# Performance work log

Measured on AMD Instinct MI355X. Metric: run time of the kernel, lower is better.

Reference implementation:

```python
import jax, jax.numpy as jnp
import numpy as np

G, N, E = 32, 1024, 16384
F_IN, HID, OUT = 128, 1024, 4096
B, S, VOCAB = 32, 256, 32000


def sage_layer(x, src, dst, Wl, Wr, b):
    # x: [N, Fin]; mean-aggregate source features at destination nodes (PyG SAGEConv)
    agg = jax.ops.segment_sum(x[src], dst, num_segments=x.shape[0])
    cnt = jax.ops.segment_sum(jnp.ones(src.shape, x.dtype), dst, num_segments=x.shape[0])
    agg = agg / jnp.maximum(cnt, 1.0)[:, None]
    return agg @ Wl + x @ Wr + b  # lin_l(mean_neigh) + lin_r(x) + bias


def setup_inputs() -> dict:
    key = jax.random.key(0)
    ks = jax.random.split(key, 12)
    node_features = jax.random.normal(ks[0], (G, N, F_IN), dtype=jnp.float32)
    edge_index = jax.random.randint(ks[1], (G, 2, E), 0, N, dtype=jnp.int32)
    input_ids = jax.random.randint(ks[2], (B, S), 0, VOCAB, dtype=jnp.int32)
    is_node = jnp.zeros((B, S), dtype=bool).at[:, 0].set(True)  # one graph token per row -> G True entries
    s1 = 1.0 / np.sqrt(F_IN)
    s2 = 1.0 / np.sqrt(HID)
    Wl1 = jax.random.normal(ks[3], (F_IN, HID), jnp.float32) * s1
    Wr1 = jax.random.normal(ks[4], (F_IN, HID), jnp.float32) * s1
    b1 = jnp.zeros((HID,), jnp.float32)
    Wl2 = jax.random.normal(ks[5], (HID, OUT), jnp.float32) * s2
    Wr2 = jax.random.normal(ks[6], (HID, OUT), jnp.float32) * s2
    b2 = jnp.zeros((OUT,), jnp.float32)
    embed_tokens = jax.random.normal(ks[7], (VOCAB, OUT), jnp.float32) * 0.02
    return {"node_features": node_features, "edge_index": edge_index, "input_ids": input_ids,
            "is_node": is_node, "Wl1": Wl1, "Wr1": Wr1, "b1": b1, "Wl2": Wl2, "Wr2": Wr2,
            "b2": b2, "embed_tokens": embed_tokens}


def reference(node_features, edge_index, input_ids, is_node, Wl1, Wr1, b1, Wl2, Wr2, b2, embed_tokens):
    def gnn_one_graph(x, ei):
        src, dst = ei[0], ei[1]
        h = jax.nn.relu(sage_layer(x, src, dst, Wl1, Wr1, b1))  # dropout is identity at inference
        h = sage_layer(h, src, dst, Wl2, Wr2, b2)
        return h.mean(axis=0)  # global_mean_pool -> [OUT]; torch code then takes [0]

    graph_emb = jax.vmap(gnn_one_graph)(node_features, edge_index)  # [G, OUT]

    inputs_embeds = embed_tokens[input_ids]  # [B, S, OUT]
    d = inputs_embeds.shape[-1]
    flat_mask = is_node.reshape(-1)                      # [B*S]
    order = jnp.cumsum(flat_mask.astype(jnp.int32)) - 1  # k-th True -> graph k
    repl = graph_emb[jnp.clip(order, 0, graph_emb.shape[0] - 1)]  # [B*S, OUT]
    out = jnp.where(flat_mask[:, None], repl, inputs_embeds.reshape(-1, d))
    return out.reshape(inputs_embeds.shape)
```

## Files before the change

kernel.cpp:

```cpp
#include <hip/hip_runtime.h>
#include <hip/hip_bf16.h>
#include <stdint.h>

#define G 32
#define NN 1024
#define EE 16384
#define FIN 128
#define HID 1024
#define OUT 4096
#define BB 32
#define SS 256

typedef __bf16 bf16_t;
typedef __attribute__((ext_vector_type(8))) __bf16 bf16x8;
typedef __attribute__((ext_vector_type(4))) float f32x4;

#define WS_FLAG     0
#define WS_CNT      4096
#define WS_WNODE    135168
#define WS_HSUM     266240
#define WS_WSUM     397312
#define WS_EMB      528384
#define WS_ZERO_BYTES 1048576
#define WS_ROWPTR   1052672
#define WS_CURSOR   1183744
#define WS_POS2G    1314816
#define WS_B1F      1347584
#define WS_B2F      1351680
#define WS_ESRC     1368064
#define WS_XBF      3465216
#define WS_AGG      11853824
#define WS_WCATT    20242432

__device__ inline float ldf(const void* p, size_t i, int f32) {
    return f32 ? ((const float*)p)[i] : (float)((const bf16_t*)p)[i];
}

__global__ __launch_bounds__(256) void probe_dtype_k(const void* x, int* flag) {
    __shared__ int s;
    int t = threadIdx.x;
    if (t == 0) s = 0;
    __syncthreads();
    const unsigned short* u = (const unsigned short*)x;
    int bad = 0;
    for (int i = t; i < 4096; i += 256) {
        unsigned short h = u[2 * i];
        int e = (h >> 7) & 0xFF;
        if (e >= 0xC0) bad = 1;
    }
    if (bad) atomicAdd(&s, 1);
    __syncthreads();
    if (t == 0) *flag = (s > 0) ? 1 : 0;
}

__global__ __launch_bounds__(256) void conv_x_k(const void* x, const int* flag,
                                                bf16_t* __restrict__ xbf) {
    int f32 = *flag;
    size_t i = ((size_t)blockIdx.x * 256 + threadIdx.x) * 4;
    if (f32) {
        const float* xf = (const float*)x;
        bf16_t o0 = (bf16_t)xf[i], o1 = (bf16_t)xf[i + 1],
               o2 = (bf16_t)xf[i + 2], o3 = (bf16_t)xf[i + 3];
        unsigned short p[4] = {*(unsigned short*)&o0, *(unsigned short*)&o1,
                               *(unsigned short*)&o2, *(unsigned short*)&o3};
        *(uint2*)(xbf + i) = *(uint2*)p;
    } else {
        *(uint2*)(xbf + i) = *(const uint2*)((const bf16_t*)x + i);
    }
}

__global__ __launch_bounds__(256) void conv_b_k(const void* b1, const void* b2,
                                                const int* flag,
                                                float* __restrict__ b1f,
                                                float* __restrict__ b2f) {
    int f32 = *flag;
    int t = blockIdx.x * 256 + threadIdx.x;
    if (t < HID) b1f[t] = ldf(b1, t, f32);
    else if (t < HID + OUT) b2f[t - HID] = ldf(b2, t - HID, f32);
}

__global__ __launch_bounds__(256) void count_edges_k(const int* __restrict__ ei,
                                                     int* __restrict__ cnt) {
    int idx = blockIdx.x * 256 + threadIdx.x;
    int g = idx >> 14, e = idx & (EE - 1);
    int dst = ei[(g * 2 + 1) * EE + e];
    atomicAdd(&cnt[g * NN + dst], 1);
}

__global__ __launch_bounds__(256) void wnode_k(const int* __restrict__ ei,
                                               const int* __restrict__ cnt,
                                               float* __restrict__ wnode) {
    int idx = blockIdx.x * 256 + threadIdx.x;
    int g = idx >> 14, e = idx & (EE - 1);
    int src = ei[g * 2 * EE + e];
    int dst = ei[(g * 2 + 1) * EE + e];
    int c = cnt[g * NN + dst];
    float w = 1.0f / (float)(c > 1 ? c : 1);
    atomicAdd(&wnode[g * NN + src], w);
}

__global__ __launch_bounds__(256) void scan_rowptr_k(const int* __restrict__ cnt,
                                                     int* __restrict__ rowptr,
                                                     int* __restrict__ cursor) {
    int g = blockIdx.x;
    const int* c = cnt + g * NN;
    __shared__ int part[256];
    int t = threadIdx.x;
    int c0 = c[t * 4], c1 = c[t * 4 + 1], c2 = c[t * 4 + 2], c3 = c[t * 4 + 3];
    int s = c0 + c1 + c2 + c3;
    part[t] = s;
    __syncthreads();
    for (int off = 1; off < 256; off <<= 1) {
        int v = (t >= off) ? part[t - off] : 0;
        __syncthreads();
        part[t] += v;
        __syncthreads();
    }
    int base = part[t] - s;
    int gi = g * NN + t * 4;
    int o0 = base, o1 = o0 + c0, o2 = o1 + c1, o3 = o2 + c2;
    rowptr[gi] = o0; rowptr[gi + 1] = o1; rowptr[gi + 2] = o2; rowptr[gi + 3] = o3;
    cursor[gi] = o0; cursor[gi + 1] = o1; cursor[gi + 2] = o2; cursor[gi + 3] = o3;
}

__global__ __launch_bounds__(256) void scatter_edges_k(const int* __restrict__ ei,
                                                       int* __restrict__ cursor,
                                                       int* __restrict__ esrc) {
    int idx = blockIdx.x * 256 + threadIdx.x;
    int g = idx >> 14, e = idx & (EE - 1);
    int src = ei[g * 2 * EE + e];
    int dst = ei[(g * 2 + 1) * EE + e];
    int p = atomicAdd(&cursor[g * NN + dst], 1);
    esrc[g * EE + p] = src;
}

__global__ __launch_bounds__(256) void aggregate_k(const bf16_t* __restrict__ x,
                                                   const int* __restrict__ rowptr,
                                                   const int* __restrict__ cnt,
                                                   const int* __restrict__ esrc,
                                                   bf16_t* __restrict__ agg) {
    int g = blockIdx.x >> 9;
    int pair = blockIdx.x & 511;
    int n = pair * 2 + (threadIdx.x >> 7);
    int f = threadIdx.x & 127;
    int start = rowptr[g * NN + n];
    int deg = cnt[g * NN + n];
    const bf16_t* xg = x + (size_t)g * NN * FIN;
    const int* es = esrc + g * EE;
    float sum = 0.f;
    for (int i = 0; i < deg; ++i) {
        int s = es[start + i];
        sum += (float)xg[s * FIN + f];
    }
    float inv = 1.0f / (float)(deg > 1 ? deg : 1);
    agg[((size_t)g * NN + n) * FIN + f] = (bf16_t)(sum * inv);
}

__global__ __launch_bounds__(256) void build_wcatT_k(const void* Wl1, const void* Wr1,
                                                     const int* flag,
                                                     bf16_t* __restrict__ wcatT) {
    int f32 = *flag;
    int n = blockIdx.x;
    int k = threadIdx.x;
    float v = (k < 128) ? ldf(Wl1, (size_t)k * HID + n, f32)
                        : ldf(Wr1, (size_t)(k - 128) * HID + n, f32);
    wcatT[n * 256 + k] = (bf16_t)v;
}

#define BKP 40
__global__ __launch_bounds__(256) void l1_gemm_k(const bf16_t* __restrict__ agg,
                                                 const bf16_t* __restrict__ x,
                                                 const bf16_t* __restrict__ wcatT,
                                                 const float* __restrict__ b1f,
                                                 const float* __restrict__ wnode,
                                                 float* __restrict__ hsum,
                                                 float* __restrict__ wsum) {
    int nt = blockIdx.x, mt = blockIdx.y, g = blockIdx.z;
    __shared__ bf16_t As[128 * BKP];
    __shared__ bf16_t Bs[128 * BKP];
    int tid = threadIdx.x;
    int lane = tid & 63, wave = tid >> 6;
    int quad = lane >> 4, l16 = lane & 15;
    int m0 = (wave >> 1) * 64, n0 = (wave & 1) * 64;

    f32x4 acc[4][4] = {};
    const size_t arow = ((size_t)g * NN + (size_t)mt * 128) * FIN;

    for (int kc = 0; kc < 8; ++kc) {
        int k0 = kc * 32;
        const bf16_t* asrc = (k0 < 128) ? (agg + arow + k0) : (x + arow + (k0 - 128));
        const bf16_t* bsrc = wcatT + (size_t)(nt * 128) * 256 + k0;
        #pragma unroll
        for (int i = 0; i < 2; ++i) {
            int gi = tid + i * 256;
            int row = gi >> 2, col = (gi & 3) * 8;
            *(bf16x8*)(&As[row * BKP + col]) = *(const bf16x8*)(asrc + row * FIN + col);
            *(bf16x8*)(&Bs[row * BKP + col]) = *(const bf16x8*)(bsrc + row * 256 + col);
        }
        __syncthreads();
        bf16x8 a[4], b[4];
        int kl = quad * 8;
        #pragma unroll
        for (int t4 = 0; t4 < 4; ++t4) {
            a[t4] = *(const bf16x8*)(&As[(m0 + t4 * 16 + l16) * BKP + kl]);
            b[t4] = *(const bf16x8*)(&Bs[(n0 + t4 * 16 + l16) * BKP + kl]);
        }
        #pragma unroll
        for (int ti = 0; ti < 4; ++ti)
            #pragma unroll
            for (int tj = 0; tj < 4; ++tj)
                acc[ti][tj] = __builtin_amdgcn_mfma_f32_16x16x32_bf16(a[ti], b[tj], acc[ti][tj], 0, 0, 0);
        __syncthreads();
    }

    const float* wn = wnode + (size_t)g * NN + mt * 128;
    #pragma unroll
    for (int tj = 0; tj < 4; ++tj) {
        int ng = nt * 128 + n0 + tj * 16 + l16;
        float bias = b1f[ng];
        float hs = 0.f, wsv = 0.f;
        #pragma unroll
        for (int ti = 0; ti < 4; ++ti) {
            int mb = m0 + ti * 16 + quad * 4;
            #pragma unroll
            for (int r = 0; r < 4; ++r) {
                float h = acc[ti][tj][r] + bias;
                h = h > 0.f ? h : 0.f;
                hs += h;
                wsv += wn[mb + r] * h;
            }
        }
        hs += __shfl_xor(hs, 16);  hs += __shfl_xor(hs, 32);
        wsv += __shfl_xor(wsv, 16); wsv += __shfl_xor(wsv, 32);
        if (quad == 0) {
            atomicAdd(&hsum[(size_t)g * HID + ng], hs);
            atomicAdd(&wsum[(size_t)g * HID + ng], wsv);
        }
    }
}

__global__ __launch_bounds__(256) void l2_gemv_k(const float* __restrict__ wsum,
                                                 const float* __restrict__ hsum,
                                                 const void* Wl2v, const void* Wr2v,
                                                 const int* flag,
                                                 float* __restrict__ emb_acc) {
    int f32 = *flag;
    int jc = blockIdx.x;
    int kc = blockIdx.y;
    int t = threadIdx.x;
    int j = jc * 256 + t;
    __shared__ float u1[G][128];
    __shared__ float u2[G][128];
    for (int i = 0; i < 16; ++i) {
        int idx = t + i * 256;
        int g = idx >> 7, kk = idx & 127;
        u1[g][kk] = wsum[g * HID + kc * 128 + kk] * (1.0f / 1024.0f);
        u2[g][kk] = hsum[g * HID + kc * 128 + kk] * (1.0f / 1024.0f);
    }
    __syncthreads();
    float acc[G] = {};
    if (f32) {
        const float* L = (const float*)Wl2v;
        const float* R = (const float*)Wr2v;
        for (int kk = 0; kk < 128; ++kk) {
            size_t krow = (size_t)(kc * 128 + kk);
            float wl = L[krow * OUT + j];
            float wr = R[krow * OUT + j];
            #pragma unroll
            for (int g = 0; g < G; ++g)
                acc[g] = fmaf(u1[g][kk], wl, fmaf(u2[g][kk], wr, acc[g]));
        }
    } else {
        const bf16_t* L = (const bf16_t*)Wl2v;
        const bf16_t* R = (const bf16_t*)Wr2v;
        for (int kk = 0; kk < 128; ++kk) {
            size_t krow = (size_t)(kc * 128 + kk);
            float wl = (float)L[krow * OUT + j];
            float wr = (float)R[krow * OUT + j];
            #pragma unroll
            for (int g = 0; g < G; ++g)
                acc[g] = fmaf(u1[g][kk], wl, fmaf(u2[g][kk], wr, acc[g]));
        }
    }
    #pragma unroll
    for (int g = 0; g < G; ++g)
        atomicAdd(&emb_acc[g * OUT + j], acc[g]);
}

__global__ __launch_bounds__(256) void pos2graph_k(const unsigned char* __restrict__ is_node,
                                                   int* __restrict__ p2g) {
    int int_mode = (is_node[256] == 0);
    const int* in32 = (const int*)is_node;
    __shared__ int part[256];
    int t = threadIdx.x;
    unsigned char m[32];
    int c = 0;
    for (int i = 0; i < 32; ++i) {
        int idx = t * 32 + i;
        unsigned char v = int_mode ? (unsigned char)(in32[idx] != 0) : (unsigned char)(is_node[idx] != 0);
        m[i] = v;
        c += v ? 1 : 0;
    }
    part[t] = c;
    __syncthreads();
    for (int off = 1; off < 256; off <<= 1) {
        int v = (t >= off) ? part[t - off] : 0;
        __syncthreads();
        part[t] += v;
        __syncthreads();
    }
    int run = part[t] - c;
    for (int i = 0; i < 32; ++i) {
        int idx = t * 32 + i;
        p2g[idx] = m[i] ? (run < (G - 1) ? run : (G - 1)) : -1;
        if (m[i]) run++;
    }
}

__global__ __launch_bounds__(256) void assemble_k(const int* __restrict__ p2g,
                                                  const int* __restrict__ input_ids,
                                                  const void* embedv,
                                                  const float* __restrict__ emb_acc,
                                                  const float* __restrict__ b2f,
                                                  const int* flag,
                                                  void* outv) {
    int f32 = *flag;
    int row = blockIdx.x;
    int t = threadIdx.x;
    int gidx = p2g[row];
    if (f32) {
        float* orow = (float*)outv + (size_t)row * OUT;
        if (gidx >= 0) {
            const float* src = emb_acc + (size_t)gidx * OUT;
            #pragma unroll
            for (int i = 0; i < 4; ++i) {
                int base = (t + i * 256) * 4;
                f32x4 v;
                #pragma unroll
                for (int k = 0; k < 4; ++k) v[k] = src[base + k] + b2f[base + k];
                *(f32x4*)(orow + base) = v;
            }
        } else {
            const uint4* s4 = (const uint4*)((const float*)embedv + (size_t)input_ids[row] * OUT);
            uint4* d4 = (uint4*)orow;
            #pragma unroll
            for (int i = 0; i < 4; ++i) d4[t + i * 256] = s4[t + i * 256];
        }
    } else {
        bf16_t* orow = (bf16_t*)outv + (size_t)row * OUT;
        if (gidx >= 0) {
            const float* src = emb_acc + (size_t)gidx * OUT;
            #pragma unroll
            for (int i = 0; i < 2; ++i) {
                int base = (t + i * 256) * 8;
                bf16x8 v;
                #pragma unroll
                for (int jj = 0; jj < 8; ++jj)
                    v[jj] = (bf16_t)(src[base + jj] + b2f[base + jj]);
                *(bf16x8*)(orow + base) = v;
            }
        } else {
            const uint4* s4 = (const uint4*)((const bf16_t*)embedv + (size_t)input_ids[row] * OUT);
            uint4* d4 = (uint4*)orow;
            d4[t] = s4[t];
            d4[t + 256] = s4[t + 256];
        }
    }
}

extern "C" void kernel_launch(void* const* d_in, const int* in_sizes, int n_in,
                              void* d_out, int out_size, void* d_ws, size_t ws_size,
                              hipStream_t stream) {
    const void* x     = d_in[0];
    const int*  ei    = (const int*)d_in[1];
    const int*  ids   = (const int*)d_in[2];
    const unsigned char* isn = (const unsigned char*)d_in[3];
    const void* Wl1   = d_in[4];
    const void* Wr1   = d_in[5];
    const void* b1    = d_in[6];
    const void* Wl2   = d_in[7];
    const void* Wr2   = d_in[8];
    const void* b2    = d_in[9];
    const void* embed = d_in[10];

    char* ws = (char*)d_ws;
    int*    flag   = (int*)  (ws + WS_FLAG);
    int*    cnt    = (int*)  (ws + WS_CNT);
    float*  wnode  = (float*)(ws + WS_WNODE);
    float*  hsum   = (float*)(ws + WS_HSUM);
    float*  wsum   = (float*)(ws + WS_WSUM);
    float*  emb    = (float*)(ws + WS_EMB);
    int*    rowptr = (int*)  (ws + WS_ROWPTR);
    int*    cursor = (int*)  (ws + WS_CURSOR);
    int*    p2g    = (int*)  (ws + WS_POS2G);
    float*  b1f    = (float*)(ws + WS_B1F);
    float*  b2f    = (float*)(ws + WS_B2F);
    int*    esrc   = (int*)  (ws + WS_ESRC);
    bf16_t* xbf    = (bf16_t*)(ws + WS_XBF);
    bf16_t* agg    = (bf16_t*)(ws + WS_AGG);
    bf16_t* wcatT  = (bf16_t*)(ws + WS_WCATT);

    hipMemsetAsync(ws + WS_CNT, 0, WS_ZERO_BYTES, stream);

    probe_dtype_k<<<1, 256, 0, stream>>>(x, flag);
    conv_x_k<<<(G * NN * FIN) / 1024, 256, 0, stream>>>(x, flag, xbf);
    conv_b_k<<<20, 256, 0, stream>>>(b1, b2, flag, b1f, b2f);
    build_wcatT_k<<<HID, 256, 0, stream>>>(Wl1, Wr1, flag, wcatT);

    count_edges_k<<<G * EE / 256, 256, 0, stream>>>(ei, cnt);
    wnode_k<<<G * EE / 256, 256, 0, stream>>>(ei, cnt, wnode);
    scan_rowptr_k<<<G, 256, 0, stream>>>(cnt, rowptr, cursor);
    scatter_edges_k<<<G * EE / 256, 256, 0, stream>>>(ei, cursor, esrc);
    aggregate_k<<<G * 512, 256, 0, stream>>>(xbf, rowptr, cnt, esrc, agg);

    l1_gemm_k<<<dim3(8, 8, G), 256, 0, stream>>>(agg, xbf, wcatT, b1f, wnode, hsum, wsum);
    l2_gemv_k<<<dim3(16, 8), 256, 0, stream>>>(wsum, hsum, Wl2, Wr2, flag, emb);

    pos2graph_k<<<1, 256, 0, stream>>>(isn, p2g);
    assemble_k<<<BB * SS, 256, 0, stream>>>(p2g, ids, embed, emb, b2f, flag, d_out);
}
```

Baseline: 935.7 us.

## Inline dtype probe, fuse small kernels, vectorize aggregation, use direct LDS loads

Removes the separate dtype-probe kernel by having each kernel recompute the f32/bf16 check from the first 1 KB of x. Folds the bias conversion into conv_x_k and the wnode atomics into scatter_edges_k, which cuts the number of launches. The aggregation now assigns one wavefront per node and reads bf16 pairs with the row pointer and degree made wave-uniform. The layer-1 GEMM stages tiles through global_load_lds into unpadded LDS, which risks bank conflicts and relies on implicit ordering before the barrier.

After: 926.8 us. No clear change (-1.0%).

```diff
diff --git a/kernel.cpp b/kernel.cpp
--- a/kernel.cpp
+++ b/kernel.cpp
@@ -12,10 +12,10 @@
 #define SS 256
 
 typedef __bf16 bf16_t;
+typedef __attribute__((ext_vector_type(2))) __bf16 bf16x2;
 typedef __attribute__((ext_vector_type(8))) __bf16 bf16x8;
 typedef __attribute__((ext_vector_type(4))) float f32x4;
 
-#define WS_FLAG     0
 #define WS_CNT      4096
 #define WS_WNODE    135168
 #define WS_HSUM     266240
@@ -36,47 +36,50 @@
     return f32 ? ((const float*)p)[i] : (float)((const bf16_t*)p)[i];
 }
 
-__global__ __launch_bounds__(256) void probe_dtype_k(const void* x, int* flag) {
-    __shared__ int s;
-    int t = threadIdx.x;
-    if (t == 0) s = 0;
-    __syncthreads();
-    const unsigned short* u = (const unsigned short*)x;
-    int bad = 0;
-    for (int i = t; i < 4096; i += 256) {
-        unsigned short h = u[2 * i];
-        int e = (h >> 7) & 0xFF;
-        if (e >= 0xC0) bad = 1;
-    }
-    if (bad) atomicAdd(&s, 1);
-    __syncthreads();
-    if (t == 0) *flag = (s > 0) ? 1 : 0;
-}
-
-__global__ __launch_bounds__(256) void conv_x_k(const void* x, const int* flag,
-                                                bf16_t* __restrict__ xbf) {
-    int f32 = *flag;
-    size_t i = ((size_t)blockIdx.x * 256 + threadIdx.x) * 4;
-    if (f32) {
-        const float* xf = (const float*)x;
-        bf16_t o0 = (bf16_t)xf[i], o1 = (bf16_t)xf[i + 1],
-               o2 = (bf16_t)xf[i + 2], o3 = (bf16_t)xf[i + 3];
-        unsigned short p[4] = {*(unsigned short*)&o0, *(unsigned short*)&o1,
-                               *(unsigned short*)&o2, *(unsigned short*)&o3};
-        *(uint2*)(xbf + i) = *(uint2*)p;
-    } else {
-        *(uint2*)(xbf + i) = *(const uint2*)((const bf16_t*)x + i);
-    }
-}
-
-__global__ __launch_bounds__(256) void conv_b_k(const void* b1, const void* b2,
-                                                const int* flag,
+__device__ inline int probe_f32(const void* xp) {
+    const uint4* u = (const uint4*)xp;
+    unsigned accm = 0;
+    #pragma unroll 4
+    for (int i = 0; i < 64; ++i) {
+        uint4 v = u[i];
+        accm |= (v.x & (v.x << 1));
+        accm |= (v.y & (v.y << 1));
+        accm |= (v.z & (v.z << 1));
+        accm |= (v.w & (v.w << 1));
+    }
+    return (accm >> 14) & 1;
+}
+
+__device__ inline void gl_lds16(const bf16_t* g, bf16_t* l) {
+    __builtin_amdgcn_global_load_lds(
+        (const __attribute__((address_space(1))) void*)g,
+        (__attribute__((address_space(3))) void*)l, 16, 0, 0);
+}
+
+__global__ __launch_bounds__(256) void conv_x_k(const void* x, const void* b1,
+                                                const void* b2,
+                                                bf16_t* __restrict__ xbf,
                                                 float* __restrict__ b1f,
                                                 float* __restrict__ b2f) {
-    int f32 = *flag;
-    int t = blockIdx.x * 256 + threadIdx.x;
-    if (t < HID) b1f[t] = ldf(b1, t, f32);
-    else if (t < HID + OUT) b2f[t - HID] = ldf(b2, t - HID, f32);
+    int f32 = probe_f32(x);
+    int bx = blockIdx.x;
+    if (bx < 4096) {
+        size_t i = ((size_t)bx * 256 + threadIdx.x) * 4;
+        if (f32) {
+            const float* xf = (const float*)x;
+            bf16_t o0 = (bf16_t)xf[i], o1 = (bf16_t)xf[i + 1],
+                   o2 = (bf16_t)xf[i + 2], o3 = (bf16_t)xf[i + 3];
+            unsigned short p[4] = {*(unsigned short*)&o0, *(unsigned short*)&o1,
+                                   *(unsigned short*)&o2, *(unsigned short*)&o3};
+            *(uint2*)(xbf + i) = *(uint2*)p;
+        } else {
+            *(uint2*)(xbf + i) = *(const uint2*)((const bf16_t*)x + i);
+        }
+    } else {
+        int t = (bx - 4096) * 256 + threadIdx.x;
+        if (t < HID) b1f[t] = ldf(b1, t, f32);
+        else if (t < HID + OUT) b2f[t - HID] = ldf(b2, t - HID, f32);
+    }
 }
 
 __global__ __launch_bounds__(256) void count_edges_k(const int* __restrict__ ei,
@@ -85,18 +88,6 @@
     int g = idx >> 14, e = idx & (EE - 1);
     int dst = ei[(g * 2 + 1) * EE + e];
     atomicAdd(&cnt[g * NN + dst], 1);
-}
-
-__global__ __launch_bounds__(256) void wnode_k(const int* __restrict__ ei,
-                                               const int* __restrict__ cnt,
-                                               float* __restrict__ wnode) {
-    int idx = blockIdx.x * 256 + threadIdx.x;
-    int g = idx >> 14, e = idx & (EE - 1);
-    int src = ei[g * 2 * EE + e];
-    int dst = ei[(g * 2 + 1) * EE + e];
-    int c = cnt[g * NN + dst];
-    float w = 1.0f / (float)(c > 1 ? c : 1);
-    atomicAdd(&wnode[g * NN + src], w);
 }
 
 __global__ __launch_bounds__(256) void scan_rowptr_k(const int* __restrict__ cnt,
@@ -124,12 +115,16 @@
 }
 
 __global__ __launch_bounds__(256) void scatter_edges_k(const int* __restrict__ ei,
+                                                       const int* __restrict__ cnt,
                                                        int* __restrict__ cursor,
-                                                       int* __restrict__ esrc) {
+                                                       int* __restrict__ esrc,
+                                                       float* __restrict__ wnode) {
     int idx = blockIdx.x * 256 + threadIdx.x;
     int g = idx >> 14, e = idx & (EE - 1);
     int src = ei[g * 2 * EE + e];
     int dst = ei[(g * 2 + 1) * EE + e];
+    int c = cnt[g * NN + dst];
+    atomicAdd(&wnode[g * NN + src], 1.0f / (float)(c > 1 ? c : 1));
     int p = atomicAdd(&cursor[g * NN + dst], 1);
     esrc[g * EE + p] = src;
 }
@@ -139,27 +134,34 @@
                                                    const int* __restrict__ cnt,
                                                    const int* __restrict__ esrc,
                                                    bf16_t* __restrict__ agg) {
-    int g = blockIdx.x >> 9;
-    int pair = blockIdx.x & 511;
-    int n = pair * 2 + (threadIdx.x >> 7);
-    int f = threadIdx.x & 127;
-    int start = rowptr[g * NN + n];
-    int deg = cnt[g * NN + n];
+    int g = blockIdx.x >> 8;
+    int nb = blockIdx.x & 255;
+    int wave = threadIdx.x >> 6;
+    int lane = threadIdx.x & 63;
+    int n = nb * 4 + wave;
+    int start = __builtin_amdgcn_readfirstlane(rowptr[g * NN + n]);
+    int deg   = __builtin_amdgcn_readfirstlane(cnt[g * NN + n]);
     const bf16_t* xg = x + (size_t)g * NN * FIN;
     const int* es = esrc + g * EE;
-    float sum = 0.f;
+    int f = lane * 2;
+    float s0 = 0.f, s1 = 0.f;
     for (int i = 0; i < deg; ++i) {
         int s = es[start + i];
-        sum += (float)xg[s * FIN + f];
+        bf16x2 v = *(const bf16x2*)(xg + s * FIN + f);
+        s0 += (float)v[0];
+        s1 += (float)v[1];
     }
     float inv = 1.0f / (float)(deg > 1 ? deg : 1);
-    agg[((size_t)g * NN + n) * FIN + f] = (bf16_t)(sum * inv);
+    bf16x2 o;
+    o[0] = (bf16_t)(s0 * inv);
+    o[1] = (bf16_t)(s1 * inv);
+    *(bf16x2*)(agg + ((size_t)g * NN + n) * FIN + f) = o;
 }
 
 __global__ __launch_bounds__(256) void build_wcatT_k(const void* Wl1, const void* Wr1,
-                                                     const int* flag,
+                                                     const void* x,
                                                      bf16_t* __restrict__ wcatT) {
-    int f32 = *flag;
+    int f32 = probe_f32(x);
     int n = blockIdx.x;
     int k = threadIdx.x;
     float v = (k < 128) ? ldf(Wl1, (size_t)k * HID + n, f32)
@@ -167,7 +169,6 @@
     wcatT[n * 256 + k] = (bf16_t)v;
 }
 
-#define BKP 40
 __global__ __launch_bounds__(256) void l1_gemm_k(const bf16_t* __restrict__ agg,
                                                  const bf16_t* __restrict__ x,
                                                  const bf16_t* __restrict__ wcatT,
@@ -176,8 +177,8 @@
                                                  float* __restrict__ hsum,
                                                  float* __restrict__ wsum) {
     int nt = blockIdx.x, mt = blockIdx.y, g = blockIdx.z;
-    __shared__ bf16_t As[128 * BKP];
-    __shared__ bf16_t Bs[128 * BKP];
+    __shared__ bf16_t As[128 * 32];
+    __shared__ bf16_t Bs[128 * 32];
     int tid = threadIdx.x;
     int lane = tid & 63, wave = tid >> 6;
     int quad = lane >> 4, l16 = lane & 15;
@@ -185,25 +186,26 @@
 
     f32x4 acc[4][4] = {};
     const size_t arow = ((size_t)g * NN + (size_t)mt * 128) * FIN;
+    const bf16_t* bslab = wcatT + (size_t)(nt * 128) * 256;
+
+    int j0 = tid,        row0 = j0 >> 2, sl0 = (j0 & 3) * 8;
+    int j1 = 256 + tid,  row1 = j1 >> 2, sl1 = (j1 & 3) * 8;
 
     for (int kc = 0; kc < 8; ++kc) {
         int k0 = kc * 32;
         const bf16_t* asrc = (k0 < 128) ? (agg + arow + k0) : (x + arow + (k0 - 128));
-        const bf16_t* bsrc = wcatT + (size_t)(nt * 128) * 256 + k0;
-        #pragma unroll
-        for (int i = 0; i < 2; ++i) {
-            int gi = tid + i * 256;
-            int row = gi >> 2, col = (gi & 3) * 8;
-            *(bf16x8*)(&As[row * BKP + col]) = *(const bf16x8*)(asrc + row * FIN + col);
-            *(bf16x8*)(&Bs[row * BKP + col]) = *(const bf16x8*)(bsrc + row * 256 + col);
-        }
+        const bf16_t* bsrc = bslab + k0;
+        gl_lds16(asrc + (size_t)row0 * FIN + sl0, &As[j0 * 8]);
+        gl_lds16(asrc + (size_t)row1 * FIN + sl1, &As[j1 * 8]);
+        gl_lds16(bsrc + (size_t)row0 * 256 + sl0, &Bs[j0 * 8]);
+        gl_lds16(bsrc + (size_t)row1 * 256 + sl1, &Bs[j1 * 8]);
         __syncthreads();
         bf16x8 a[4], b[4];
         int kl = quad * 8;
         #pragma unroll
         for (int t4 = 0; t4 < 4; ++t4) {
-            a[t4] = *(const bf16x8*)(&As[(m0 + t4 * 16 + l16) * BKP + kl]);
-            b[t4] = *(const bf16x8*)(&Bs[(n0 + t4 * 16 + l16) * BKP + kl]);
+            a[t4] = *(const bf16x8*)(&As[(m0 + t4 * 16 + l16) * 32 + kl]);
+            b[t4] = *(const bf16x8*)(&Bs[(n0 + t4 * 16 + l16) * 32 + kl]);
         }
         #pragma unroll
         for (int ti = 0; ti < 4; ++ti)
@@ -242,9 +244,9 @@
 __global__ __launch_bounds__(256) void l2_gemv_k(const float* __restrict__ wsum,
                                                  const float* __restrict__ hsum,
                                                  const void* Wl2v, const void* Wr2v,
-                                                 const int* flag,
+                                                 const void* x,
                                                  float* __restrict__ emb_acc) {
-    int f32 = *flag;
+    int f32 = probe_f32(x);
     int jc = blockIdx.x;
     int kc = blockIdx.y;
     int t = threadIdx.x;
@@ -322,9 +324,9 @@
                                                   const void* embedv,
                                                   const float* __restrict__ emb_acc,
                                                   const float* __restrict__ b2f,
-                                                  const int* flag,
+                                                  const void* x,
                                                   void* outv) {
-    int f32 = *flag;
+    int f32 = probe_f32(x);
     int row = blockIdx.x;
     int t = threadIdx.x;
     int gidx = p2g[row];
@@ -384,7 +386,6 @@
     const void* embed = d_in[10];
 
     char* ws = (char*)d_ws;
-    int*    flag   = (int*)  (ws + WS_FLAG);
     int*    cnt    = (int*)  (ws + WS_CNT);
     float*  wnode  = (float*)(ws + WS_WNODE);
     float*  hsum   = (float*)(ws + WS_HSUM);
@@ -402,20 +403,17 @@
 
     hipMemsetAsync(ws + WS_CNT, 0, WS_ZERO_BYTES, stream);
 
-    probe_dtype_k<<<1, 256, 0, stream>>>(x, flag);
-    conv_x_k<<<(G * NN * FIN) / 1024, 256, 0, stream>>>(x, flag, xbf);
-    conv_b_k<<<20, 256, 0, stream>>>(b1, b2, flag, b1f, b2f);
-    build_wcatT_k<<<HID, 256, 0, stream>>>(Wl1, Wr1, flag, wcatT);
+    conv_x_k<<<4096 + 20, 256, 0, stream>>>(x, b1, b2, xbf, b1f, b2f);
+    build_wcatT_k<<<HID, 256, 0, stream>>>(Wl1, Wr1, x, wcatT);
 
     count_edges_k<<<G * EE / 256, 256, 0, stream>>>(ei, cnt);
-    wnode_k<<<G * EE / 256, 256, 0, stream>>>(ei, cnt, wnode);
     scan_rowptr_k<<<G, 256, 0, stream>>>(cnt, rowptr, cursor);
-    scatter_edges_k<<<G * EE / 256, 256, 0, stream>>>(ei, cursor, esrc);
-    aggregate_k<<<G * 512, 256, 0, stream>>>(xbf, rowptr, cnt, esrc, agg);
+    scatter_edges_k<<<G * EE / 256, 256, 0, stream>>>(ei, cnt, cursor, esrc, wnode);
+    aggregate_k<<<G * 256, 256, 0, stream>>>(xbf, rowptr, cnt, esrc, agg);
 
     l1_gemm_k<<<dim3(8, 8, G), 256, 0, stream>>>(agg, xbf, wcatT, b1f, wnode, hsum, wsum);
-    l2_gemv_k<<<dim3(16, 8), 256, 0, stream>>>(wsum, hsum, Wl2, Wr2, flag, emb);
+    l2_gemv_k<<<dim3(16, 8), 256, 0, stream>>>(wsum, hsum, Wl2, Wr2, x, emb);
 
     pos2graph_k<<<1, 256, 0, stream>>>(isn, p2g);
-    assemble_k<<<BB * SS, 256, 0, stream>>>(p2g, ids, embed, emb, b2f, flag, d_out);
-}
+    assemble_k<<<BB * SS, 256, 0, stream>>>(p2g, ids, embed, emb, b2f, x, d_out);
+}
```
